# Optimization experiments

Hardware: AMD Instinct MI355X
Metric: run time of the kernel (lower is better)

Reference implementation:

```python
import jax, jax.numpy as jnp
import numpy as np

H = 1024       # hidden_size
NH = 16        # num_heads
HD = H // NH   # head_dim
I = 4096       # intermediate_size
EPS = 1e-6


def setup_inputs() -> dict:
    key = jax.random.key(0)
    ks = jax.random.split(key, 10)
    s = 0.02
    return {
        "hidden_states": jax.random.normal(ks[0], (8, 1025, H), jnp.float32),
        "qkv_w": jax.random.normal(ks[1], (3 * H, H), jnp.float32) * s,
        "qkv_b": jnp.zeros((3 * H,), jnp.float32),
        "proj_w": jax.random.normal(ks[2], (H, H), jnp.float32) * s,
        "proj_b": jnp.zeros((H,), jnp.float32),
        "fc1_w": jax.random.normal(ks[3], (I, H), jnp.float32) * s,
        "fc1_b": jnp.zeros((I,), jnp.float32),
        "fc2_w": jax.random.normal(ks[4], (H, I), jnp.float32) * s,
        "fc2_b": jnp.zeros((H,), jnp.float32),
        "norm1_w": jnp.ones((H,), jnp.float32),
        "norm1_b": jnp.zeros((H,), jnp.float32),
        "norm2_w": jnp.ones((H,), jnp.float32),
        "norm2_b": jnp.zeros((H,), jnp.float32),
        "ls1": jnp.ones((H,), jnp.float32),
        "ls2": jnp.ones((H,), jnp.float32),
    }


def _layer_norm(x, w, b):
    mu = jnp.mean(x, axis=-1, keepdims=True)
    var = jnp.mean(jnp.square(x - mu), axis=-1, keepdims=True)
    return (x - mu) * jax.lax.rsqrt(var + EPS) * w + b


def _attention(x, qkv_w, qkv_b, proj_w, proj_b):
    B, N, _ = x.shape
    qkv = x @ qkv_w.T + qkv_b                       # [B,N,3H]
    qkv = qkv.reshape(B, N, 3, NH, HD)
    q, k, v = qkv[:, :, 0], qkv[:, :, 1], qkv[:, :, 2]  # [B,N,NH,HD]
    scale = HD ** -0.5
    scores = jnp.einsum("bqhd,bkhd->bhqk", q, k) * scale
    attn = jax.nn.softmax(scores, axis=-1)
    out = jnp.einsum("bhqk,bkhd->bqhd", attn, v).reshape(B, N, H)
    return out @ proj_w.T + proj_b


def _mlp(x, fc1_w, fc1_b, fc2_w, fc2_b):
    h = jax.nn.gelu(x @ fc1_w.T + fc1_b, approximate=False)
    return h @ fc2_w.T + fc2_b


def reference(hidden_states, qkv_w, qkv_b, proj_w, proj_b, fc1_w, fc1_b,
              fc2_w, fc2_b, norm1_w, norm1_b, norm2_w, norm2_b, ls1, ls2):
    x = hidden_states
    x = x + ls1 * _attention(_layer_norm(x, norm1_w, norm1_b),
                             qkv_w, qkv_b, proj_w, proj_b)
    x = x + ls2 * _mlp(_layer_norm(x, norm2_w, norm2_b),
                       fc1_w, fc1_b, fc2_w, fc2_b)
    return x
```

## Files before the change

### kernel.cpp

```cpp
#include <hip/hip_runtime.h>
#include <cstdint>
#include <cstddef>

typedef __bf16 bf16;
typedef __bf16 bf16x8 __attribute__((ext_vector_type(8)));
typedef __bf16 bf16x4 __attribute__((ext_vector_type(4)));
typedef float  floatx4 __attribute__((ext_vector_type(4)));

#define MFMA16(a,b,c) __builtin_amdgcn_mfma_f32_16x16x32_bf16((a),(b),(c),0,0,0)

__device__ __forceinline__ void async_copy16(void* lds, const void* g) {
    __builtin_amdgcn_global_load_lds(
        (const __attribute__((address_space(1))) unsigned int*)g,
        (__attribute__((address_space(3))) unsigned int*)lds,
        16, 0, 0);
}

__global__ __launch_bounds__(256) void cvt_kernel(const float* __restrict__ src,
                                                  bf16* __restrict__ dst) {
    const int i = blockIdx.x * 256 + threadIdx.x;
    const float4 v = ((const float4*)src)[i];
    bf16x4 o;
    o[0] = (bf16)v.x; o[1] = (bf16)v.y; o[2] = (bf16)v.z; o[3] = (bf16)v.w;
    ((bf16x4*)dst)[i] = o;
}

__global__ __launch_bounds__(256) void ln_kernel(const float* __restrict__ x,
                                                 const float* __restrict__ w,
                                                 const float* __restrict__ b,
                                                 bf16* __restrict__ out) {
    const int row = blockIdx.x;
    const int t = threadIdx.x;
    const float4 v = ((const float4*)(x + (size_t)row * 1024))[t];
    float s  = v.x + v.y + v.z + v.w;
    float ss = v.x*v.x + v.y*v.y + v.z*v.z + v.w*v.w;
#pragma unroll
    for (int m = 32; m >= 1; m >>= 1) {
        s  += __shfl_xor(s,  m, 64);
        ss += __shfl_xor(ss, m, 64);
    }
    __shared__ float red[8];
    const int wave = t >> 6, lane = t & 63;
    if (lane == 0) { red[wave] = s; red[4 + wave] = ss; }
    __syncthreads();
    s  = red[0] + red[1] + red[2] + red[3];
    ss = red[4] + red[5] + red[6] + red[7];
    const float mean = s * (1.0f / 1024.0f);
    const float var  = ss * (1.0f / 1024.0f) - mean * mean;
    const float inv  = rsqrtf(var + 1e-6f);
    const float4 wv = ((const float4*)w)[t];
    const float4 bv = ((const float4*)b)[t];
    bf16x4 o;
    o[0] = (bf16)((v.x - mean) * inv * wv.x + bv.x);
    o[1] = (bf16)((v.y - mean) * inv * wv.y + bv.y);
    o[2] = (bf16)((v.z - mean) * inv * wv.z + bv.z);
    o[3] = (bf16)((v.w - mean) * inv * wv.w + bv.w);
    *(bf16x4*)(out + (size_t)row * 1024 + t * 4) = o;
}

template <int EPI>
__global__ __launch_bounds__(256, 3) void gemm_bt(
    const bf16* __restrict__ A, const bf16* __restrict__ B,
    const float* __restrict__ bias, void* __restrict__ Cout,
    const float* __restrict__ res, const float* __restrict__ lsv,
    int M, int N, int K) {
    __shared__ bf16 sA[128 * 64];
    __shared__ bf16 sB[128 * 64];
    const int tid  = threadIdx.x;
    const int wave = tid >> 6;
    const int lane = tid & 63;
    const int lrow = lane & 15;
    const int quad = lane >> 4;
    const int nx   = gridDim.x;
    const int lin  = blockIdx.y * nx + blockIdx.x;
    const int w    = nx >> 3;
    const int xcd  = lin & 7;
    const int slot = lin >> 3;
    const int ntile = xcd * w + (slot % w);
    const int mtile = slot / w;
    const int m0 = mtile * 128;
    const int n0 = ntile * 128;
    const int wm = (wave >> 1) * 64;
    const int wn = (wave & 1) * 64;

    floatx4 acc[4][4] = {};

    const int srow  = tid >> 3;
    const int spart = (tid & 7) ^ (srow & 7);
    const bf16* Ag[4];
    const bf16* Bg[4];
#pragma unroll
    for (int c = 0; c < 4; c++) {
        int am = m0 + c * 32 + srow; if (am > M - 1) am = M - 1;
        Ag[c] = A + (size_t)am * K + spart * 8;
        Bg[c] = B + (size_t)(n0 + c * 32 + srow) * K + spart * 8;
    }
    const int sswz = lrow & 7;

    for (int kk = 0; kk < K; kk += 64) {
        __syncthreads();
#pragma unroll
        for (int c = 0; c < 4; c++) {
            async_copy16(&sA[(c * 256 + wave * 64) * 8], Ag[c] + kk);
            async_copy16(&sB[(c * 256 + wave * 64) * 8], Bg[c] + kk);
        }
        __syncthreads();
#pragma unroll
        for (int kq = 0; kq < 2; kq++) {
            const int so = ((kq * 4 + quad) ^ sswz) * 8;
            bf16x8 af[4], bfr[4];
#pragma unroll
            for (int i = 0; i < 4; i++)
                af[i] = *(const bf16x8*)&sA[(wm + i * 16 + lrow) * 64 + so];
#pragma unroll
            for (int j = 0; j < 4; j++)
                bfr[j] = *(const bf16x8*)&sB[(wn + j * 16 + lrow) * 64 + so];
#pragma unroll
            for (int i = 0; i < 4; i++)
#pragma unroll
                for (int j = 0; j < 4; j++)
                    acc[i][j] = MFMA16(af[i], bfr[j], acc[i][j]);
        }
    }

    const int nb = n0 + wn + lrow;
#pragma unroll
    for (int i = 0; i < 4; i++) {
        const int mb = m0 + wm + i * 16 + quad * 4;
#pragma unroll
        for (int r = 0; r < 4; r++) {
            const int m = mb + r;
            if (m < M) {
#pragma unroll
                for (int j = 0; j < 4; j++) {
                    const int n = nb + j * 16;
                    float v = acc[i][j][r] + bias[n];
                    if constexpr (EPI == 0) {
                        ((bf16*)Cout)[(size_t)m * N + n] = (bf16)v;
                    } else if constexpr (EPI == 2) {
                        const float s_ = v * (0.7978845608f + 0.0356774081f * v * v);
                        const float e2s = __builtin_amdgcn_exp2f(2.8853900817779268f * s_);
                        const float g = v * (1.0f - __builtin_amdgcn_rcpf(1.0f + e2s));
                        ((bf16*)Cout)[(size_t)m * N + n] = (bf16)g;
                    } else {
                        ((float*)Cout)[(size_t)m * N + n] =
                            res[(size_t)m * N + n] + lsv[n] * v;
                    }
                }
            }
        }
    }
}

__global__ __launch_bounds__(256) void transpose_v(const bf16* __restrict__ qkv,
                                                   bf16* __restrict__ vt) {
    const int tt = blockIdx.x;
    const int bh = blockIdx.y;
    const int b = bh >> 4, h = bh & 15;
    __shared__ bf16 tile[64][72];
    const int t = threadIdx.x;
    const int tok0 = tt * 64;
#pragma unroll
    for (int i = 0; i < 4; i++) {
        const int idx4 = i * 256 + t;
        const int tl = idx4 >> 4;
        const int d4 = (idx4 & 15) * 4;
        const int tok = tok0 + tl;
        bf16x4 val;
        val[0] = (bf16)0.0f; val[1] = (bf16)0.0f; val[2] = (bf16)0.0f; val[3] = (bf16)0.0f;
        if (tok <= 1024) {
            val = *(const bf16x4*)(qkv + ((size_t)(b * 1025 + tok)) * 3072 + 2048 + h * 64 + d4);
        }
        tile[d4 + 0][tl] = val[0];
        tile[d4 + 1][tl] = val[1];
        tile[d4 + 2][tl] = val[2];
        tile[d4 + 3][tl] = val[3];
    }
    __syncthreads();
#pragma unroll
    for (int i = 0; i < 4; i++) {
        const int idx4 = i * 256 + t;
        const int d = idx4 >> 4;
        const int t4 = (idx4 & 15) * 4;
        bf16x4 o;
        o[0] = tile[d][t4 + 0]; o[1] = tile[d][t4 + 1];
        o[2] = tile[d][t4 + 2]; o[3] = tile[d][t4 + 3];
        *(bf16x4*)(vt + ((size_t)bh * 64 + d) * 1152 + tok0 + t4) = o;
    }
}

__global__ __launch_bounds__(256, 3) void attn_kernel(const bf16* __restrict__ qkv,
                                                      const bf16* __restrict__ vt,
                                                      bf16* __restrict__ o_out) {
    const int qt = blockIdx.x;
    const int bh = blockIdx.y;
    const int b = bh >> 4, h = bh & 15;
    __shared__ bf16 sK[2 * 128 * 32];
    __shared__ bf16 sV[4 * 64 * 32];
    __shared__ bf16 sQP[4 * 16 * 136];
    const int tid = threadIdx.x, wave = tid >> 6, lane = tid & 63;
    const int lrow = lane & 15, quad = lane >> 4, lko = quad * 8;
    const float cexp = 0.18033688011112042f;
    const size_t row0 = (size_t)b * 1025;

#pragma unroll
    for (int i = 0; i < 2; i++) {
        const int g = i * 256 + tid;
        const int ks = g >> 8, rr = (g >> 2) & 63, p = g & 3;
        int qrow = qt * 64 + rr; if (qrow > 1024) qrow = 1024;
        async_copy16(&sQP[(i * 256 + wave * 64) * 8],
                     qkv + (row0 + qrow) * 3072 + h * 64 + ks * 32 + p * 8);
    }
    __syncthreads();
    bf16x8 qf[2];
    qf[0] = *(const bf16x8*)&sQP[(wave * 16 + lrow) * 32 + lko];
    qf[1] = *(const bf16x8*)&sQP[2048 + (wave * 16 + lrow) * 32 + lko];
#pragma unroll
    for (int i = 0; i < 8; i++) {
        qf[0][i] = (bf16)((float)qf[0][i] * cexp);
        qf[1][i] = (bf16)((float)qf[1][i] * cexp);
    }
    bf16x8 ones;
#pragma unroll
    for (int i = 0; i < 8; i++) ones[i] = (bf16)1.0f;

    floatx4 o[4] = {};
    floatx4 ol = {};
    bf16* pw = &sQP[wave * (16 * 136)];

    for (int ktile = 0; ktile < 9; ++ktile) {
        const int kt0 = ktile * 128;
        __syncthreads();
#pragma unroll
        for (int i = 0; i < 4; i++) {
            const int g = i * 256 + tid;
            const int ks = g >> 9, tok = (g >> 2) & 127, p = g & 3;
            int krow = kt0 + tok; if (krow > 1024) krow = 1024;
            async_copy16(&sK[(i * 256 + wave * 64) * 8],
                         qkv + (row0 + krow) * 3072 + 1024 + h * 64 + ks * 32 + p * 8);
        }
#pragma unroll
        for (int i = 0; i < 4; i++) {
            const int g = i * 256 + tid;
            const int kc = g >> 8, d = (g >> 2) & 63, p = g & 3;
            async_copy16(&sV[(i * 256 + wave * 64) * 8],
                         vt + ((size_t)bh * 64 + d) * 1152 + kt0 + kc * 32 + p * 8);
        }
        __syncthreads();

        const bool lastTile = (ktile == 8);
#pragma unroll
        for (int nt = 0; nt < 8; nt++) {
            bf16x8 k0 = *(const bf16x8*)&sK[(nt * 16 + lrow) * 32 + lko];
            bf16x8 k1 = *(const bf16x8*)&sK[4096 + (nt * 16 + lrow) * 32 + lko];
            floatx4 z = {};
            z = MFMA16(k0, qf[0], z);
            z = MFMA16(k1, qf[1], z);
            bf16x4 pb;
#pragma unroll
            for (int r = 0; r < 4; r++) {
                float p = __builtin_amdgcn_exp2f(z[r]);
                if (lastTile) {
                    const int ktok = kt0 + nt * 16 + quad * 4 + r;
                    p = (ktok <= 1024) ? p : 0.0f;
                }
                pb[r] = (bf16)p;
            }
            *(bf16x4*)&pw[lrow * 136 + nt * 16 + quad * 4] = pb;
        }
#pragma unroll
        for (int ks = 0; ks < 4; ks++) {
            bf16x8 pa = *(const bf16x8*)&pw[lrow * 136 + ks * 32 + lko];
#pragma unroll
            for (int j = 0; j < 4; j++) {
                bf16x8 vb = *(const bf16x8*)&sV[ks * 2048 + (j * 16 + lrow) * 32 + lko];
                o[j] = MFMA16(pa, vb, o[j]);
            }
            ol = MFMA16(pa, ones, ol);
        }
    }

#pragma unroll
    for (int r = 0; r < 4; r++) {
        const int q = qt * 64 + wave * 16 + quad * 4 + r;
        if (q <= 1024) {
            const float inv = 1.0f / ol[r];
            const size_t orow = (row0 + q) * 1024 + h * 64;
#pragma unroll
            for (int j = 0; j < 4; j++)
                o_out[orow + j * 16 + lrow] = (bf16)(o[j][r] * inv);
        }
    }
}

extern "C" void kernel_launch(void* const* d_in, const int* in_sizes, int n_in,
                              void* d_out, int out_size, void* d_ws, size_t ws_size,
                              hipStream_t stream) {
    const float* x      = (const float*)d_in[0];
    const float* qkv_w  = (const float*)d_in[1];
    const float* qkv_b  = (const float*)d_in[2];
    const float* proj_w = (const float*)d_in[3];
    const float* proj_b = (const float*)d_in[4];
    const float* fc1_w  = (const float*)d_in[5];
    const float* fc1_b  = (const float*)d_in[6];
    const float* fc2_w  = (const float*)d_in[7];
    const float* fc2_b  = (const float*)d_in[8];
    const float* n1w    = (const float*)d_in[9];
    const float* n1b    = (const float*)d_in[10];
    const float* n2w    = (const float*)d_in[11];
    const float* n2b    = (const float*)d_in[12];
    const float* ls1    = (const float*)d_in[13];
    const float* ls2    = (const float*)d_in[14];

    char* ws = (char*)d_ws;
    bf16*  wqkv  = (bf16*)(ws + 0);
    bf16*  wproj = (bf16*)(ws + 6291456);
    bf16*  wfc1  = (bf16*)(ws + 8388608);
    bf16*  wfc2  = (bf16*)(ws + 16777216);
    bf16*  vt    = (bf16*)(ws + 25165824);
    bf16*  attnO = (bf16*)(ws + 44040192);
    float* x1    = (float*)(ws + 60833792);
    bf16*  lnbuf = (bf16*)(ws + 94420992);
    bf16*  big   = (bf16*)(ws + 111214592);

    const int M = 8200;

    cvt_kernel<<<3072, 256, 0, stream>>>(qkv_w, wqkv);
    cvt_kernel<<<1024, 256, 0, stream>>>(proj_w, wproj);
    cvt_kernel<<<4096, 256, 0, stream>>>(fc1_w, wfc1);
    cvt_kernel<<<4096, 256, 0, stream>>>(fc2_w, wfc2);

    ln_kernel<<<M, 256, 0, stream>>>(x, n1w, n1b, lnbuf);
    gemm_bt<0><<<dim3(24, 65), 256, 0, stream>>>(lnbuf, wqkv, qkv_b, (void*)big,
                                                 nullptr, nullptr, M, 3072, 1024);
    transpose_v<<<dim3(17, 128), 256, 0, stream>>>(big, vt);
    attn_kernel<<<dim3(17, 128), 256, 0, stream>>>(big, vt, attnO);
    gemm_bt<1><<<dim3(8, 65), 256, 0, stream>>>(attnO, wproj, proj_b, (void*)x1,
                                                x, ls1, M, 1024, 1024);
    ln_kernel<<<M, 256, 0, stream>>>(x1, n2w, n2b, lnbuf);
    gemm_bt<2><<<dim3(32, 65), 256, 0, stream>>>(lnbuf, wfc1, fc1_b, (void*)big,
                                                 nullptr, nullptr, M, 4096, 1024);
    gemm_bt<3><<<dim3(8, 65), 256, 0, stream>>>(big, wfc2, fc2_b, d_out,
                                                x1, ls2, M, 1024, 4096);
}
```

Before: 505.7 us.

## Fuse weight casts, shrink attention key tile, remap N=1024 GEMM blocks into M strips

Merges the four weight-conversion launches into one kernel that picks its source by block index, removing launch overhead. The attention kernel now walks 64-key tiles instead of 128, cutting LDS use and raising launch bounds to 4 blocks per CU, at the cost of more loop iterations and barriers. The proj and fc2 GEMMs (N=1024) use a new block mapping where each blockIdx.x covers a strip of 9 consecutive M tiles for one N tile, aiming for better A-tile locality per XCD; it pads the grid and early-exits out-of-range tiles.

Result: no change. 505.8 us (+0.0%).

```diff
diff --git a/kernel.cpp b/kernel.cpp
--- a/kernel.cpp
+++ b/kernel.cpp
@@ -16,9 +16,21 @@
         16, 0, 0);
 }
 
-__global__ __launch_bounds__(256) void cvt_kernel(const float* __restrict__ src,
-                                                  bf16* __restrict__ dst) {
-    const int i = blockIdx.x * 256 + threadIdx.x;
+__global__ __launch_bounds__(256) void cvt_all(const float* __restrict__ s0,
+                                               const float* __restrict__ s1,
+                                               const float* __restrict__ s2,
+                                               const float* __restrict__ s3,
+                                               bf16* __restrict__ d0,
+                                               bf16* __restrict__ d1,
+                                               bf16* __restrict__ d2,
+                                               bf16* __restrict__ d3) {
+    const int blk = blockIdx.x;
+    const float* src; bf16* dst; int base;
+    if (blk < 3072)      { src = s0; dst = d0; base = blk; }
+    else if (blk < 4096) { src = s1; dst = d1; base = blk - 3072; }
+    else if (blk < 8192) { src = s2; dst = d2; base = blk - 4096; }
+    else                 { src = s3; dst = d3; base = blk - 8192; }
+    const int i = base * 256 + threadIdx.x;
     const float4 v = ((const float4*)src)[i];
     bf16x4 o;
     o[0] = (bf16)v.x; o[1] = (bf16)v.y; o[2] = (bf16)v.z; o[3] = (bf16)v.w;
@@ -58,12 +70,12 @@
     *(bf16x4*)(out + (size_t)row * 1024 + t * 4) = o;
 }
 
-template <int EPI>
+template <int EPI, bool MSTRIP>
 __global__ __launch_bounds__(256, 3) void gemm_bt(
     const bf16* __restrict__ A, const bf16* __restrict__ B,
     const float* __restrict__ bias, void* __restrict__ Cout,
     const float* __restrict__ res, const float* __restrict__ lsv,
-    int M, int N, int K) {
+    int M, int N, int K, int mt_per) {
     __shared__ bf16 sA[128 * 64];
     __shared__ bf16 sB[128 * 64];
     const int tid  = threadIdx.x;
@@ -71,15 +83,24 @@
     const int lane = tid & 63;
     const int lrow = lane & 15;
     const int quad = lane >> 4;
-    const int nx   = gridDim.x;
-    const int lin  = blockIdx.y * nx + blockIdx.x;
-    const int w    = nx >> 3;
-    const int xcd  = lin & 7;
-    const int slot = lin >> 3;
-    const int ntile = xcd * w + (slot % w);
-    const int mtile = slot / w;
-    const int m0 = mtile * 128;
-    const int n0 = ntile * 128;
+    int m0, n0;
+    if constexpr (MSTRIP) {
+        const int mtile = blockIdx.x * mt_per + blockIdx.y % mt_per;
+        const int ntile = blockIdx.y / mt_per;
+        m0 = mtile * 128;
+        n0 = ntile * 128;
+        if (m0 >= M) return;
+    } else {
+        const int nx   = gridDim.x;
+        const int lin  = blockIdx.y * nx + blockIdx.x;
+        const int w    = nx >> 3;
+        const int xcd  = lin & 7;
+        const int slot = lin >> 3;
+        const int ntile = xcd * w + (slot % w);
+        const int mtile = slot / w;
+        m0 = mtile * 128;
+        n0 = ntile * 128;
+    }
     const int wm = (wave >> 1) * 64;
     const int wn = (wave & 1) * 64;
 
@@ -189,15 +210,15 @@
     }
 }
 
-__global__ __launch_bounds__(256, 3) void attn_kernel(const bf16* __restrict__ qkv,
+__global__ __launch_bounds__(256, 4) void attn_kernel(const bf16* __restrict__ qkv,
                                                       const bf16* __restrict__ vt,
                                                       bf16* __restrict__ o_out) {
     const int qt = blockIdx.x;
     const int bh = blockIdx.y;
     const int b = bh >> 4, h = bh & 15;
-    __shared__ bf16 sK[2 * 128 * 32];
-    __shared__ bf16 sV[4 * 64 * 32];
-    __shared__ bf16 sQP[4 * 16 * 136];
+    __shared__ bf16 sK[2 * 64 * 32];
+    __shared__ bf16 sV[2 * 64 * 32];
+    __shared__ bf16 sQP[4 * 16 * 72];
     const int tid = threadIdx.x, wave = tid >> 6, lane = tid & 63;
     const int lrow = lane & 15, quad = lane >> 4, lko = quad * 8;
     const float cexp = 0.18033688011112042f;
@@ -226,21 +247,21 @@
 
     floatx4 o[4] = {};
     floatx4 ol = {};
-    bf16* pw = &sQP[wave * (16 * 136)];
-
-    for (int ktile = 0; ktile < 9; ++ktile) {
-        const int kt0 = ktile * 128;
+    bf16* pw = &sQP[wave * (16 * 72)];
+
+    for (int ktile = 0; ktile < 17; ++ktile) {
+        const int kt0 = ktile * 64;
         __syncthreads();
 #pragma unroll
-        for (int i = 0; i < 4; i++) {
+        for (int i = 0; i < 2; i++) {
             const int g = i * 256 + tid;
-            const int ks = g >> 9, tok = (g >> 2) & 127, p = g & 3;
+            const int ks = g >> 8, tok = (g >> 2) & 63, p = g & 3;
             int krow = kt0 + tok; if (krow > 1024) krow = 1024;
             async_copy16(&sK[(i * 256 + wave * 64) * 8],
                          qkv + (row0 + krow) * 3072 + 1024 + h * 64 + ks * 32 + p * 8);
         }
 #pragma unroll
-        for (int i = 0; i < 4; i++) {
+        for (int i = 0; i < 2; i++) {
             const int g = i * 256 + tid;
             const int kc = g >> 8, d = (g >> 2) & 63, p = g & 3;
             async_copy16(&sV[(i * 256 + wave * 64) * 8],
@@ -248,11 +269,11 @@
         }
         __syncthreads();
 
-        const bool lastTile = (ktile == 8);
-#pragma unroll
-        for (int nt = 0; nt < 8; nt++) {
+        const bool lastTile = (ktile == 16);
+#pragma unroll
+        for (int nt = 0; nt < 4; nt++) {
             bf16x8 k0 = *(const bf16x8*)&sK[(nt * 16 + lrow) * 32 + lko];
-            bf16x8 k1 = *(const bf16x8*)&sK[4096 + (nt * 16 + lrow) * 32 + lko];
+            bf16x8 k1 = *(const bf16x8*)&sK[2048 + (nt * 16 + lrow) * 32 + lko];
             floatx4 z = {};
             z = MFMA16(k0, qf[0], z);
             z = MFMA16(k1, qf[1], z);
@@ -266,11 +287,11 @@
                 }
                 pb[r] = (bf16)p;
             }
-            *(bf16x4*)&pw[lrow * 136 + nt * 16 + quad * 4] = pb;
-        }
-#pragma unroll
-        for (int ks = 0; ks < 4; ks++) {
-            bf16x8 pa = *(const bf16x8*)&pw[lrow * 136 + ks * 32 + lko];
+            *(bf16x4*)&pw[lrow * 72 + nt * 16 + quad * 4] = pb;
+        }
+#pragma unroll
+        for (int ks = 0; ks < 2; ks++) {
+            bf16x8 pa = *(const bf16x8*)&pw[lrow * 72 + ks * 32 + lko];
 #pragma unroll
             for (int j = 0; j < 4; j++) {
                 bf16x8 vb = *(const bf16x8*)&sV[ks * 2048 + (j * 16 + lrow) * 32 + lko];
@@ -325,21 +346,19 @@
 
     const int M = 8200;
 
-    cvt_kernel<<<3072, 256, 0, stream>>>(qkv_w, wqkv);
-    cvt_kernel<<<1024, 256, 0, stream>>>(proj_w, wproj);
-    cvt_kernel<<<4096, 256, 0, stream>>>(fc1_w, wfc1);
-    cvt_kernel<<<4096, 256, 0, stream>>>(fc2_w, wfc2);
+    cvt_all<<<12288, 256, 0, stream>>>(qkv_w, proj_w, fc1_w, fc2_w,
+                                       wqkv, wproj, wfc1, wfc2);
 
     ln_kernel<<<M, 256, 0, stream>>>(x, n1w, n1b, lnbuf);
-    gemm_bt<0><<<dim3(24, 65), 256, 0, stream>>>(lnbuf, wqkv, qkv_b, (void*)big,
-                                                 nullptr, nullptr, M, 3072, 1024);
+    gemm_bt<0, false><<<dim3(24, 65), 256, 0, stream>>>(lnbuf, wqkv, qkv_b, (void*)big,
+                                                        nullptr, nullptr, M, 3072, 1024, 0);
     transpose_v<<<dim3(17, 128), 256, 0, stream>>>(big, vt);
     attn_kernel<<<dim3(17, 128), 256, 0, stream>>>(big, vt, attnO);
-    gemm_bt<1><<<dim3(8, 65), 256, 0, stream>>>(attnO, wproj, proj_b, (void*)x1,
-                                                x, ls1, M, 1024, 1024);
+    gemm_bt<1, true><<<dim3(8, 72), 256, 0, stream>>>(attnO, wproj, proj_b, (void*)x1,
+                                                      x, ls1, M, 1024, 1024, 9);
     ln_kernel<<<M, 256, 0, stream>>>(x1, n2w, n2b, lnbuf);
-    gemm_bt<2><<<dim3(32, 65), 256, 0, stream>>>(lnbuf, wfc1, fc1_b, (void*)big,
-                                                 nullptr, nullptr, M, 4096, 1024);
-    gemm_bt<3><<<dim3(8, 65), 256, 0, stream>>>(big, wfc2, fc2_b, d_out,
-                                                x1, ls2, M, 1024, 4096);
-}
+    gemm_bt<2, false><<<dim3(32, 65), 256, 0, stream>>>(lnbuf, wfc1, fc1_b, (void*)big,
+                                                        nullptr, nullptr, M, 4096, 1024, 0);
+    gemm_bt<3, true><<<dim3(8, 72), 256, 0, stream>>>(big, wfc2, fc2_b, d_out,
+                                                      x1, ls2, M, 1024, 4096, 9);
+}
```
